# Kernel optimization log

Measured on AMD Instinct MI355X. Metric: run time of the kernel, lower is better.

## Reference

```python
import jax, jax.numpy as jnp
import numpy as np

B, S, E, H, L = 8, 1024, 1024, 16, 2
D = E // H
EPS = 1e-5
THRESH = 0.5


def layer_norm(x, g, b):
    mu = x.mean(-1, keepdims=True)
    var = ((x - mu) ** 2).mean(-1, keepdims=True)
    return (x - mu) * jax.lax.rsqrt(var + EPS) * g + b


def mha(x, w_in, w_out):
    # x: [B,S,E]; w_in: [3E,E]; w_out: [E,E] (no biases, PyTorch MultiheadAttention bias=False)
    qkv = x @ w_in.T  # [B,S,3E]
    q, k, v = jnp.split(qkv, 3, axis=-1)
    q = q.reshape(q.shape[0], q.shape[1], H, D).transpose(0, 2, 1, 3)
    k = k.reshape(k.shape[0], k.shape[1], H, D).transpose(0, 2, 1, 3)
    v = v.reshape(v.shape[0], v.shape[1], H, D).transpose(0, 2, 1, 3)
    scores = jnp.einsum('bhqd,bhkd->bhqk', q, k) / jnp.sqrt(jnp.float32(D)).astype(x.dtype)
    attn = jax.nn.softmax(scores, axis=-1)
    out = jnp.einsum('bhqk,bhkd->bhqd', attn, v)
    out = out.transpose(0, 2, 1, 3).reshape(x.shape[0], x.shape[1], E)
    return out @ w_out.T


def thinking_layer(x, w_in, w_out, ffn1, ffn2, g1, b1, g2, b2):
    x = layer_norm(x + mha(x, w_in, w_out), g1, b1)
    h = jax.nn.gelu(x @ ffn1.T, approximate=False) @ ffn2.T
    return layer_norm(x + h, g2, b2)


def setup_inputs() -> dict:
    key = jax.random.key(0)
    ks = jax.random.split(key, 8)
    s = jnp.float32(0.02)
    return {
        'x': jax.random.normal(ks[0], (B, S, E), jnp.float32),
        'w_in': jax.random.normal(ks[1], (L, 3 * E, E), jnp.float32) * s,
        'w_out': jax.random.normal(ks[2], (L, E, E), jnp.float32) * s,
        'ffn_w1': jax.random.normal(ks[3], (L, 4 * E, E), jnp.float32) * s,
        'ffn_w2': jax.random.normal(ks[4], (L, E, 4 * E), jnp.float32) * s,
        'ln1_g': jnp.ones((L, E), jnp.float32),
        'ln1_b': jnp.zeros((L, E), jnp.float32),
        'ln2_g': jnp.ones((L, E), jnp.float32),
        'ln2_b': jnp.zeros((L, E), jnp.float32),
        'ce_w1': jax.random.normal(ks[5], (E // 4, E), jnp.float32) * s,
        'ce_b1': jnp.zeros((E // 4,), jnp.float32),
        'ce_w2': jax.random.normal(ks[6], (1, E // 4), jnp.float32) * s,
        'ce_b2': jnp.zeros((1,), jnp.float32),
        'fast_w': jax.random.normal(ks[7], (E, E), jnp.float32) * s,
    }


def reference(x, w_in, w_out, ffn_w1, ffn_w2, ln1_g, ln1_b, ln2_g, ln2_b,
              ce_w1, ce_b1, ce_w2, ce_b2, fast_w):
    # complexity estimator: mean-pool -> MLP -> logit per batch element
    pooled = x.mean(axis=1)                                   # [B,E]
    h = jax.nn.relu(pooled @ ce_w1.T + ce_b1)                 # [B,E/4]
    logits = (h @ ce_w2.T + ce_b2).squeeze(-1)                # [B]
    probs = jax.nn.sigmoid(logits)
    mode = (probs > THRESH)                                   # eval-mode deterministic routing

    # thinking path (System 2): L stacked attention+FFN layers
    t = x
    for i in range(L):
        t = thinking_layer(t, w_in[i], w_out[i], ffn_w1[i], ffn_w2[i],
                           ln1_g[i], ln1_b[i], ln2_g[i], ln2_b[i])

    # fast path (System 1)
    fast = jax.nn.gelu(x @ fast_w.T, approximate=False)

    out = jnp.where(mode[:, None, None], t, fast)
    mode_f = mode.astype(x.dtype)
    return out, probs, mode_f, mode_f.mean()
```

## Files before the change

kernel.cpp:

```cpp
#include <hip/hip_runtime.h>
#include <cstdint>
#include <cstddef>

#define Bsz 8
#define Ssz 1024
#define Esz 1024
#define Hn  16
#define Dh  64
#define OUT_PROBS 8388608
#define OUT_MODE  8388616
#define OUT_MEAN  8388624

typedef unsigned short u16;
typedef __attribute__((ext_vector_type(8))) __bf16 bf16x8;
typedef __attribute__((ext_vector_type(4))) float  floatx4;

__device__ __forceinline__ float bf2f(u16 u){ return __uint_as_float(((unsigned)u)<<16); }
__device__ __forceinline__ u16 f2bf(float f){
  unsigned u = __float_as_uint(f);
  u += 0x7fffu + ((u>>16)&1u);
  return (u16)(u>>16);
}
__device__ __forceinline__ void unpack2(unsigned u, float& lo, float& hi){
  lo = __uint_as_float(u<<16);
  hi = __uint_as_float(u & 0xffff0000u);
}
__device__ __forceinline__ unsigned pack2(float lo, float hi){
  return (unsigned)f2bf(lo) | ((unsigned)f2bf(hi)<<16);
}
__device__ __forceinline__ void async16(const void* g, void* l){
  __builtin_amdgcn_global_load_lds((const __attribute__((address_space(1))) void*)g,
                                   (__attribute__((address_space(3))) void*)l, 16, 0, 0);
}
__device__ __forceinline__ float gelu_exact(float x){
  return 0.5f*x*(1.0f + erff(x*0.70710678118654752f));
}

__global__ __launch_bounds__(256)
void f2b_kernel(const float* __restrict__ src, u16* __restrict__ dst, int n8)
{
  const int i = blockIdx.x*256 + threadIdx.x;
  if(i >= n8) return;
  float4 a = ((const float4*)src)[2*i];
  float4 b = ((const float4*)src)[2*i+1];
  uint4 w;
  w.x = pack2(a.x, a.y); w.y = pack2(a.z, a.w);
  w.z = pack2(b.x, b.y); w.w = pack2(b.z, b.w);
  ((uint4*)dst)[i] = w;
}

template<int EPI, int SKIP>
__global__ __launch_bounds__(256, 2)
void gemm_bt(const u16* __restrict__ A, const u16* __restrict__ W,
             void* __restrict__ Cv, const u16* __restrict__ R,
             const float* __restrict__ modes, int N, int K)
{
  const int m0 = blockIdx.x * 128;
  if(SKIP == 1 && modes[m0 >> 10] == 0.0f) return;
  if(SKIP == 2 && modes[m0 >> 10] != 0.0f) return;

  __shared__ __align__(16) u16 AsLo[128*32];
  __shared__ __align__(16) u16 AsHi[128*32];
  __shared__ __align__(16) u16 BsLo[128*32];
  __shared__ __align__(16) u16 BsHi[128*32];

  const int tid  = threadIdx.x;
  const int wave = tid >> 6;
  const int lane = tid & 63;
  const int q    = lane >> 4;
  const int r16  = lane & 15;
  const int wm   = (wave >> 1) * 64;
  const int wn   = (wave & 1) * 64;
  const int n0   = blockIdx.y * 128;

  floatx4 acc[4][4];
  #pragma unroll
  for(int i=0;i<4;i++)
    #pragma unroll
    for(int j=0;j<4;j++){ floatx4 z = {0.f,0.f,0.f,0.f}; acc[i][j] = z; }

  const int row0 = tid >> 2;
  const int kc   = (tid & 3) * 8;

  for(int k0 = 0; k0 < K; k0 += 64){
    __syncthreads();
    async16(A + (size_t)(m0 + row0     )*K + k0 + kc,      AsLo + wave*512);
    async16(A + (size_t)(m0 + row0 + 64)*K + k0 + kc,      AsLo + 2048 + wave*512);
    async16(A + (size_t)(m0 + row0     )*K + k0 + 32 + kc, AsHi + wave*512);
    async16(A + (size_t)(m0 + row0 + 64)*K + k0 + 32 + kc, AsHi + 2048 + wave*512);
    async16(W + (size_t)(n0 + row0     )*K + k0 + kc,      BsLo + wave*512);
    async16(W + (size_t)(n0 + row0 + 64)*K + k0 + kc,      BsLo + 2048 + wave*512);
    async16(W + (size_t)(n0 + row0     )*K + k0 + 32 + kc, BsHi + wave*512);
    async16(W + (size_t)(n0 + row0 + 64)*K + k0 + 32 + kc, BsHi + 2048 + wave*512);
    __syncthreads();

    {
      bf16x8 af[4], bfr[4];
      #pragma unroll
      for(int i=0;i<4;i++){
        af[i]  = *(const bf16x8*)&AsLo[(wm + i*16 + r16)*32 + q*8];
        bfr[i] = *(const bf16x8*)&BsLo[(wn + i*16 + r16)*32 + q*8];
      }
      #pragma unroll
      for(int i=0;i<4;i++)
        #pragma unroll
        for(int j=0;j<4;j++)
          acc[i][j] = __builtin_amdgcn_mfma_f32_16x16x32_bf16(af[i], bfr[j], acc[i][j], 0, 0, 0);
    }
    {
      bf16x8 af[4], bfr[4];
      #pragma unroll
      for(int i=0;i<4;i++){
        af[i]  = *(const bf16x8*)&AsHi[(wm + i*16 + r16)*32 + q*8];
        bfr[i] = *(const bf16x8*)&BsHi[(wn + i*16 + r16)*32 + q*8];
      }
      #pragma unroll
      for(int i=0;i<4;i++)
        #pragma unroll
        for(int j=0;j<4;j++)
          acc[i][j] = __builtin_amdgcn_mfma_f32_16x16x32_bf16(af[i], bfr[j], acc[i][j], 0, 0, 0);
    }
  }

  #pragma unroll
  for(int i=0;i<4;i++){
    const int row = m0 + wm + i*16 + q*4;
    #pragma unroll
    for(int j=0;j<4;j++){
      const int col = n0 + wn + j*16 + r16;
      #pragma unroll
      for(int r=0;r<4;r++){
        float v = acc[i][j][r];
        const size_t idx = (size_t)(row + r)*N + col;
        if(EPI == 1) v += bf2f(R[idx]);
        if(EPI == 2 || EPI == 3) v = gelu_exact(v);
        if(EPI == 3) ((float*)Cv)[idx] = v;
        else         ((u16*)Cv)[idx] = f2bf(v);
      }
    }
  }
}

#define PSTR 136
__global__ __launch_bounds__(256, 2)
void attn_kernel(const u16* __restrict__ qkv, u16* __restrict__ out,
                 const float* __restrict__ modes)
{
  const int bh = blockIdx.x & 127;
  const int b  = bh >> 4;
  if(modes[b] == 0.0f) return;

  __shared__ __align__(16) u16 Qs[2*64*32];
  __shared__ __align__(16) u16 Ks[2*128*32];
  __shared__ __align__(16) u16 Vt[64*PSTR];
  __shared__ __align__(16) u16 Ps[64*PSTR];
  __shared__ float lsump[2][64];

  const int tid = threadIdx.x;
  const int w   = tid >> 6;
  const int lane= tid & 63;
  const int q   = lane >> 4;
  const int r16 = lane & 15;

  const int qt = blockIdx.x >> 7;
  const int h  = bh & 15;
  const int q0 = qt * 64;

  const u16* qbase = qkv + (size_t)(b*Ssz)*3072;

  {
    const int r = tid >> 2;
    const int c = (tid & 3) * 8;
    #pragma unroll
    for(int half=0; half<2; half++)
      async16(qbase + (size_t)(q0 + r)*3072 + h*64 + half*32 + c,
              &Qs[half*2048 + w*512]);
  }

  const int wm  = (w >> 1) * 32;
  const int wnS = (w & 1) * 64;
  const int wnO = (w & 1) * 32;

  floatx4 acc_o[2][2];
  #pragma unroll
  for(int i=0;i<2;i++)
    #pragma unroll
    for(int j=0;j<2;j++){ floatx4 z={0.f,0.f,0.f,0.f}; acc_o[i][j]=z; }
  float ps[2][4] = {{0.f,0.f,0.f,0.f},{0.f,0.f,0.f,0.f}};

  for(int ck=0; ck<8; ck++){
    const int k0 = ck*128;
    __syncthreads();
    {
      const int r = tid >> 2;
      const int c = (tid & 3) * 8;
      #pragma unroll
      for(int half=0; half<2; half++)
        #pragma unroll
        for(int g=0; g<2; g++)
          async16(qbase + (size_t)(k0 + g*64 + r)*3072 + 1024 + h*64 + half*32 + c,
                  &Ks[half*4096 + g*2048 + w*512]);
    }
    {
      const int kp = tid >> 2;
      const int dg = tid & 3;
      const uint4* v0 = (const uint4*)(qbase + (size_t)(k0 + 2*kp    )*3072 + 2048 + h*64 + dg*16);
      const uint4* v1 = (const uint4*)(qbase + (size_t)(k0 + 2*kp + 1)*3072 + 2048 + h*64 + dg*16);
      uint4 a0 = v0[0], a1 = v0[1], b0 = v1[0], b1 = v1[1];
      unsigned wa[8] = {a0.x,a0.y,a0.z,a0.w,a1.x,a1.y,a1.z,a1.w};
      unsigned wb[8] = {b0.x,b0.y,b0.z,b0.w,b1.x,b1.y,b1.z,b1.w};
      unsigned* vt32 = (unsigned*)Vt;
      #pragma unroll
      for(int u=0; u<8; u++){
        const int d = dg*16 + u*2;
        vt32[(size_t)d*68 + kp]     = (wa[u] & 0xffffu) | (wb[u] << 16);
        vt32[(size_t)(d+1)*68 + kp] = (wa[u] >> 16) | (wb[u] & 0xffff0000u);
      }
    }
    __syncthreads();

    floatx4 accS[2][4];
    #pragma unroll
    for(int i=0;i<2;i++)
      #pragma unroll
      for(int j=0;j<4;j++){ floatx4 z={0.f,0.f,0.f,0.f}; accS[i][j]=z; }
    #pragma unroll
    for(int half=0; half<2; half++){
      bf16x8 af[2], bf[4];
      #pragma unroll
      for(int i=0;i<2;i++)
        af[i] = *(const bf16x8*)&Qs[half*2048 + (wm + i*16 + r16)*32 + q*8];
      #pragma unroll
      for(int j=0;j<4;j++)
        bf[j] = *(const bf16x8*)&Ks[half*4096 + (wnS + j*16 + r16)*32 + q*8];
      #pragma unroll
      for(int i=0;i<2;i++)
        #pragma unroll
        for(int j=0;j<4;j++)
          accS[i][j] = __builtin_amdgcn_mfma_f32_16x16x32_bf16(af[i], bf[j], accS[i][j], 0,0,0);
    }
    #pragma unroll
    for(int i=0;i<2;i++)
      #pragma unroll
      for(int j=0;j<4;j++)
        #pragma unroll
        for(int r=0;r<4;r++){
          const float p = __expf(accS[i][j][r] * 0.125f);
          ps[i][r] += p;
          Ps[(size_t)(wm + i*16 + q*4 + r)*PSTR + wnS + j*16 + r16] = f2bf(p);
        }
    __syncthreads();

    #pragma unroll
    for(int ks=0; ks<4; ks++){
      bf16x8 ap[2], bp[2];
      #pragma unroll
      for(int i=0;i<2;i++)
        ap[i] = *(const bf16x8*)&Ps[(size_t)(wm + i*16 + r16)*PSTR + ks*32 + q*8];
      #pragma unroll
      for(int j=0;j<2;j++)
        bp[j] = *(const bf16x8*)&Vt[(size_t)(wnO + j*16 + r16)*PSTR + ks*32 + q*8];
      #pragma unroll
      for(int i=0;i<2;i++)
        #pragma unroll
        for(int j=0;j<2;j++)
          acc_o[i][j] = __builtin_amdgcn_mfma_f32_16x16x32_bf16(ap[i], bp[j], acc_o[i][j], 0,0,0);
    }
  }

  #pragma unroll
  for(int i=0;i<2;i++)
    #pragma unroll
    for(int r=0;r<4;r++){
      float v = ps[i][r];
      v += __shfl_xor(v, 1, 64);
      v += __shfl_xor(v, 2, 64);
      v += __shfl_xor(v, 4, 64);
      v += __shfl_xor(v, 8, 64);
      ps[i][r] = v;
    }
  if(r16 == 0){
    #pragma unroll
    for(int i=0;i<2;i++)
      #pragma unroll
      for(int r=0;r<4;r++)
        lsump[w & 1][wm + i*16 + q*4 + r] = ps[i][r];
  }
  __syncthreads();

  #pragma unroll
  for(int i=0;i<2;i++)
    #pragma unroll
    for(int r=0;r<4;r++){
      const int row = wm + i*16 + q*4 + r;
      const float inv = 1.0f / (lsump[0][row] + lsump[1][row]);
      #pragma unroll
      for(int j=0;j<2;j++){
        const int col = h*64 + wnO + j*16 + r16;
        out[(size_t)(b*Ssz + q0 + row)*Esz + col] = f2bf(acc_o[i][j][r] * inv);
      }
    }
}

template<int FIN>
__global__ __launch_bounds__(256)
void ln_kernel(const u16* __restrict__ X, const float* __restrict__ G,
               const float* __restrict__ Bi, u16* __restrict__ Y,
               const float* __restrict__ modes, float* __restrict__ outp)
{
  const int row = blockIdx.x;
  if(modes[row >> 10] == 0.0f) return;
  const int tid = threadIdx.x;
  const int wave = tid >> 6, lane = tid & 63;

  uint2 u = ((const uint2*)(X + (size_t)row*Esz))[tid];
  float x0,x1,x2,x3;
  unpack2(u.x, x0, x1); unpack2(u.y, x2, x3);
  float s  = x0+x1+x2+x3;
  float ss = x0*x0 + x1*x1 + x2*x2 + x3*x3;
  #pragma unroll
  for(int off=32; off; off>>=1){
    s  += __shfl_down(s,  off, 64);
    ss += __shfl_down(ss, off, 64);
  }
  __shared__ float rs[4], rss[4], bc[2];
  if(lane == 0){ rs[wave] = s; rss[wave] = ss; }
  __syncthreads();
  if(tid == 0){
    float S  = rs[0]+rs[1]+rs[2]+rs[3];
    float SS = rss[0]+rss[1]+rss[2]+rss[3];
    float mu  = S * (1.0f/1024.0f);
    float var = SS * (1.0f/1024.0f) - mu*mu;
    bc[0] = mu; bc[1] = 1.0f/sqrtf(var + 1e-5f);
  }
  __syncthreads();
  const float mu = bc[0], inv = bc[1];
  float4 g4 = ((const float4*)G)[tid];
  float4 b4 = ((const float4*)Bi)[tid];
  if(FIN){
    float4 o;
    o.x = (x0-mu)*inv*g4.x + b4.x;
    o.y = (x1-mu)*inv*g4.y + b4.y;
    o.z = (x2-mu)*inv*g4.z + b4.z;
    o.w = (x3-mu)*inv*g4.w + b4.w;
    ((float4*)(outp + (size_t)row*Esz))[tid] = o;
  } else {
    uint2 w;
    w.x = pack2((x0-mu)*inv*g4.x + b4.x, (x1-mu)*inv*g4.y + b4.y);
    w.y = pack2((x2-mu)*inv*g4.z + b4.z, (x3-mu)*inv*g4.w + b4.w);
    ((uint2*)(Y + (size_t)row*Esz))[tid] = w;
  }
}

__global__ __launch_bounds__(256)
void pool1_kernel(const float* __restrict__ x, float* __restrict__ part)
{
  const int b = blockIdx.x, tc = blockIdx.y;
  const int e4 = threadIdx.x;
  const float* p = x + (size_t)(b*Ssz + tc*32)*Esz + e4*4;
  float4 s = {0.f,0.f,0.f,0.f};
  for(int t=0; t<32; t++){
    float4 v = *(const float4*)(p + (size_t)t*Esz);
    s.x += v.x; s.y += v.y; s.z += v.z; s.w += v.w;
  }
  ((float4*)(part + (size_t)(b*32 + tc)*Esz))[e4] = s;
}

__global__ void ce1_kernel(const float* __restrict__ part, const float* __restrict__ w1,
                           const float* __restrict__ b1, float* __restrict__ hbuf)
{
  __shared__ float pl[1024];
  const int b = blockIdx.x, n = threadIdx.x;
  for(int i = threadIdx.x; i < 1024; i += 256){
    float s = 0.f;
    for(int tc=0; tc<32; tc++) s += part[(size_t)(b*32 + tc)*Esz + i];
    pl[i] = s * (1.0f/1024.0f);
  }
  __syncthreads();
  const float* wr = w1 + (size_t)n*1024;
  float s = 0.f;
  for(int k=0; k<1024; k++) s += pl[k]*wr[k];
  s += b1[n];
  hbuf[b*256 + n] = fmaxf(s, 0.f);
}

__global__ void ce2_kernel(const float* __restrict__ hbuf, const float* __restrict__ w2,
                           const float* __restrict__ b2, float* __restrict__ modes,
                           float* __restrict__ outp)
{
  const int tid = threadIdx.x;
  const int b = tid >> 5, i = tid & 31;
  float s = 0.f;
  for(int k=i; k<256; k+=32) s += hbuf[b*256 + k] * w2[k];
  #pragma unroll
  for(int off=16; off; off>>=1) s += __shfl_down(s, off, 32);
  __shared__ float md[8];
  if(i == 0){
    const float logit = s + b2[0];
    const float prob = 1.0f/(1.0f + expf(-logit));
    const float m = prob > 0.5f ? 1.0f : 0.0f;
    modes[b] = m; md[b] = m;
    outp[OUT_PROBS + b] = prob;
    outp[OUT_MODE  + b] = m;
  }
  __syncthreads();
  if(tid == 0){
    float acc = 0.f;
    for(int k=0;k<8;k++) acc += md[k];
    outp[OUT_MEAN] = acc * 0.125f;
  }
}

extern "C" void kernel_launch(void* const* d_in, const int* in_sizes, int n_in,
                              void* d_out, int out_size, void* d_ws, size_t ws_size,
                              hipStream_t stream)
{
  const float* x      = (const float*)d_in[0];
  const float* w_in   = (const float*)d_in[1];
  const float* w_out  = (const float*)d_in[2];
  const float* ffn_w1 = (const float*)d_in[3];
  const float* ffn_w2 = (const float*)d_in[4];
  const float* ln1_g  = (const float*)d_in[5];
  const float* ln1_b  = (const float*)d_in[6];
  const float* ln2_g  = (const float*)d_in[7];
  const float* ln2_b  = (const float*)d_in[8];
  const float* ce_w1  = (const float*)d_in[9];
  const float* ce_b1  = (const float*)d_in[10];
  const float* ce_w2  = (const float*)d_in[11];
  const float* ce_b2  = (const float*)d_in[12];
  const float* fast_w = (const float*)d_in[13];
  float* out = (float*)d_out;

  u16* x_bf     = (u16*)d_ws;
  u16* w_in_bf  = x_bf    + (size_t)8192*1024;
  u16* w_out_bf = w_in_bf + (size_t)2*3072*1024;
  u16* ffn1_bf  = w_out_bf+ (size_t)2*1024*1024;
  u16* ffn2_bf  = ffn1_bf + (size_t)2*4096*1024;
  u16* fast_bf  = ffn2_bf + (size_t)2*1024*4096;
  u16* big      = fast_bf + (size_t)1024*1024;
  u16* attn     = big     + (size_t)8192*4096;
  u16* resid    = attn    + (size_t)8192*1024;
  u16* bufA     = resid   + (size_t)8192*1024;
  u16* bufB     = bufA    + (size_t)8192*1024;
  float* part   = (float*)(bufB + (size_t)8192*1024);
  float* hbuf   = part + (size_t)8*32*1024;
  float* modes  = hbuf + 2048;
  const size_t need = (size_t)((char*)(modes + 8) - (char*)d_ws);
  if(ws_size < need) return;

  u16* qkv  = big;
  u16* hmid = big;

  f2b_kernel<<<4096, 256, 0, stream>>>(x,      x_bf,     8192*1024/8);
  f2b_kernel<<<3072, 256, 0, stream>>>(w_in,   w_in_bf,  2*3072*1024/8);
  f2b_kernel<<<1024, 256, 0, stream>>>(w_out,  w_out_bf, 2*1024*1024/8);
  f2b_kernel<<<4096, 256, 0, stream>>>(ffn_w1, ffn1_bf,  2*4096*1024/8);
  f2b_kernel<<<4096, 256, 0, stream>>>(ffn_w2, ffn2_bf,  2*4096*1024/8);
  f2b_kernel<<< 512, 256, 0, stream>>>(fast_w, fast_bf,  1024*1024/8);

  pool1_kernel<<<dim3(8,32), 256, 0, stream>>>(x, part);
  ce1_kernel<<<8, 256, 0, stream>>>(part, ce_w1, ce_b1, hbuf);
  ce2_kernel<<<1, 256, 0, stream>>>(hbuf, ce_w2, ce_b2, modes, out);

  const u16* t = x_bf;
  for(int l=0; l<2; l++){
    gemm_bt<0,1><<<dim3(64,24), 256, 0, stream>>>(t, w_in_bf + (size_t)l*3072*1024, qkv, nullptr, modes, 3072, 1024);
    attn_kernel<<<2048, 256, 0, stream>>>(qkv, attn, modes);
    gemm_bt<1,1><<<dim3(64, 8), 256, 0, stream>>>(attn, w_out_bf + (size_t)l*1024*1024, resid, t, modes, 1024, 1024);
    ln_kernel<0><<<8192, 256, 0, stream>>>(resid, ln1_g + l*1024, ln1_b + l*1024, bufA, modes, nullptr);
    gemm_bt<2,1><<<dim3(64,32), 256, 0, stream>>>(bufA, ffn1_bf + (size_t)l*4096*1024, hmid, nullptr, modes, 4096, 1024);
    gemm_bt<1,1><<<dim3(64, 8), 256, 0, stream>>>(hmid, ffn2_bf + (size_t)l*1024*4096, resid, bufA, modes, 1024, 4096);
    if(l == 0)
      ln_kernel<0><<<8192, 256, 0, stream>>>(resid, ln2_g + l*1024, ln2_b + l*1024, bufB, modes, nullptr);
    else
      ln_kernel<1><<<8192, 256, 0, stream>>>(resid, ln2_g + l*1024, ln2_b + l*1024, nullptr, modes, out);
    t = bufB;
  }

  gemm_bt<3,2><<<dim3(64, 8), 256, 0, stream>>>(x_bf, fast_bf, out, nullptr, modes, 1024, 1024);
}
```

Measured before the change: 958.7 us.

## Shrink attention key tile, hoist Q fragments, and batch fp32-to-bf16 conversions

The attention kernel now processes keys in 64-row chunks instead of 128, with smaller shared K/V/P buffers. It also keeps Q fragments in registers across the loop and raises launch bounds to 4 blocks per CU for higher occupancy. The six separate fp32-to-bf16 conversion launches are merged into a single multi-segment kernel to cut launch overhead. The trade-off is twice as many loop iterations and barriers in attention, and a per-thread segment lookup in the conversion kernel.

After: 913.9 us. 4.7% less time.

```diff
diff --git a/kernel.cpp b/kernel.cpp
--- a/kernel.cpp
+++ b/kernel.cpp
@@ -36,17 +36,26 @@
   return 0.5f*x*(1.0f + erff(x*0.70710678118654752f));
 }
 
+struct F2B {
+  const float* s[6];
+  u16* d[6];
+  unsigned end[6];
+};
+
 __global__ __launch_bounds__(256)
-void f2b_kernel(const float* __restrict__ src, u16* __restrict__ dst, int n8)
-{
-  const int i = blockIdx.x*256 + threadIdx.x;
-  if(i >= n8) return;
-  float4 a = ((const float4*)src)[2*i];
-  float4 b = ((const float4*)src)[2*i+1];
+void f2b_multi(F2B p)
+{
+  const unsigned i = blockIdx.x*256 + threadIdx.x;
+  int k = 0;
+  #pragma unroll
+  for(int t=0; t<5; t++) if(i >= p.end[t]) k = t+1;
+  const unsigned j = i - (k ? p.end[k-1] : 0);
+  float4 a = ((const float4*)p.s[k])[2*j];
+  float4 b = ((const float4*)p.s[k])[2*j+1];
   uint4 w;
   w.x = pack2(a.x, a.y); w.y = pack2(a.z, a.w);
   w.z = pack2(b.x, b.y); w.w = pack2(b.z, b.w);
-  ((uint4*)dst)[i] = w;
+  ((uint4*)p.d[k])[j] = w;
 }
 
 template<int EPI, int SKIP>
@@ -141,8 +150,9 @@
   }
 }
 
-#define PSTR 136
-__global__ __launch_bounds__(256, 2)
+#define VSTR 68
+#define PSTR 72
+__global__ __launch_bounds__(256, 4)
 void attn_kernel(const u16* __restrict__ qkv, u16* __restrict__ out,
                  const float* __restrict__ modes)
 {
@@ -151,8 +161,8 @@
   if(modes[b] == 0.0f) return;
 
   __shared__ __align__(16) u16 Qs[2*64*32];
-  __shared__ __align__(16) u16 Ks[2*128*32];
-  __shared__ __align__(16) u16 Vt[64*PSTR];
+  __shared__ __align__(16) u16 Ks[2*64*32];
+  __shared__ __align__(16) u16 Vt[64*VSTR];
   __shared__ __align__(16) u16 Ps[64*PSTR];
   __shared__ float lsump[2][64];
 
@@ -168,18 +178,25 @@
 
   const u16* qbase = qkv + (size_t)(b*Ssz)*3072;
 
-  {
-    const int r = tid >> 2;
-    const int c = (tid & 3) * 8;
-    #pragma unroll
-    for(int half=0; half<2; half++)
-      async16(qbase + (size_t)(q0 + r)*3072 + h*64 + half*32 + c,
-              &Qs[half*2048 + w*512]);
-  }
+  const int sr = tid >> 2;
+  const int sc = (tid & 3) * 8;
+
+  #pragma unroll
+  for(int half=0; half<2; half++)
+    async16(qbase + (size_t)(q0 + sr)*3072 + h*64 + half*32 + sc,
+            &Qs[half*2048 + w*512]);
+  __syncthreads();
 
   const int wm  = (w >> 1) * 32;
-  const int wnS = (w & 1) * 64;
+  const int wnS = (w & 1) * 32;
   const int wnO = (w & 1) * 32;
+
+  bf16x8 qf[2][2];
+  #pragma unroll
+  for(int half=0; half<2; half++)
+    #pragma unroll
+    for(int i=0;i<2;i++)
+      qf[half][i] = *(const bf16x8*)&Qs[half*2048 + (wm + i*16 + r16)*32 + q*8];
 
   floatx4 acc_o[2][2];
   #pragma unroll
@@ -188,61 +205,52 @@
     for(int j=0;j<2;j++){ floatx4 z={0.f,0.f,0.f,0.f}; acc_o[i][j]=z; }
   float ps[2][4] = {{0.f,0.f,0.f,0.f},{0.f,0.f,0.f,0.f}};
 
-  for(int ck=0; ck<8; ck++){
-    const int k0 = ck*128;
+  const int kp = tid & 31;
+  const int dg = tid >> 5;
+
+  for(int ck=0; ck<16; ck++){
+    const int k0 = ck*64;
     __syncthreads();
+    #pragma unroll
+    for(int half=0; half<2; half++)
+      async16(qbase + (size_t)(k0 + sr)*3072 + 1024 + h*64 + half*32 + sc,
+              &Ks[half*2048 + w*512]);
     {
-      const int r = tid >> 2;
-      const int c = (tid & 3) * 8;
-      #pragma unroll
-      for(int half=0; half<2; half++)
-        #pragma unroll
-        for(int g=0; g<2; g++)
-          async16(qbase + (size_t)(k0 + g*64 + r)*3072 + 1024 + h*64 + half*32 + c,
-                  &Ks[half*4096 + g*2048 + w*512]);
-    }
-    {
-      const int kp = tid >> 2;
-      const int dg = tid & 3;
-      const uint4* v0 = (const uint4*)(qbase + (size_t)(k0 + 2*kp    )*3072 + 2048 + h*64 + dg*16);
-      const uint4* v1 = (const uint4*)(qbase + (size_t)(k0 + 2*kp + 1)*3072 + 2048 + h*64 + dg*16);
-      uint4 a0 = v0[0], a1 = v0[1], b0 = v1[0], b1 = v1[1];
-      unsigned wa[8] = {a0.x,a0.y,a0.z,a0.w,a1.x,a1.y,a1.z,a1.w};
-      unsigned wb[8] = {b0.x,b0.y,b0.z,b0.w,b1.x,b1.y,b1.z,b1.w};
+      const uint4 va = *(const uint4*)(qbase + (size_t)(k0 + 2*kp    )*3072 + 2048 + h*64 + dg*8);
+      const uint4 vb = *(const uint4*)(qbase + (size_t)(k0 + 2*kp + 1)*3072 + 2048 + h*64 + dg*8);
+      unsigned wa[4] = {va.x,va.y,va.z,va.w};
+      unsigned wb[4] = {vb.x,vb.y,vb.z,vb.w};
       unsigned* vt32 = (unsigned*)Vt;
       #pragma unroll
-      for(int u=0; u<8; u++){
-        const int d = dg*16 + u*2;
-        vt32[(size_t)d*68 + kp]     = (wa[u] & 0xffffu) | (wb[u] << 16);
-        vt32[(size_t)(d+1)*68 + kp] = (wa[u] >> 16) | (wb[u] & 0xffff0000u);
+      for(int u=0; u<4; u++){
+        const int d0 = dg*8 + 2*u;
+        vt32[(size_t)d0*34 + kp]     = (wa[u] & 0xffffu) | (wb[u] << 16);
+        vt32[(size_t)(d0+1)*34 + kp] = (wa[u] >> 16) | (wb[u] & 0xffff0000u);
       }
     }
     __syncthreads();
 
-    floatx4 accS[2][4];
+    floatx4 accS[2][2];
     #pragma unroll
     for(int i=0;i<2;i++)
       #pragma unroll
-      for(int j=0;j<4;j++){ floatx4 z={0.f,0.f,0.f,0.f}; accS[i][j]=z; }
+      for(int j=0;j<2;j++){ floatx4 z={0.f,0.f,0.f,0.f}; accS[i][j]=z; }
     #pragma unroll
     for(int half=0; half<2; half++){
-      bf16x8 af[2], bf[4];
-      #pragma unroll
-      for(int i=0;i<2;i++)
-        af[i] = *(const bf16x8*)&Qs[half*2048 + (wm + i*16 + r16)*32 + q*8];
-      #pragma unroll
-      for(int j=0;j<4;j++)
-        bf[j] = *(const bf16x8*)&Ks[half*4096 + (wnS + j*16 + r16)*32 + q*8];
+      bf16x8 bf[2];
+      #pragma unroll
+      for(int j=0;j<2;j++)
+        bf[j] = *(const bf16x8*)&Ks[half*2048 + (wnS + j*16 + r16)*32 + q*8];
       #pragma unroll
       for(int i=0;i<2;i++)
         #pragma unroll
-        for(int j=0;j<4;j++)
-          accS[i][j] = __builtin_amdgcn_mfma_f32_16x16x32_bf16(af[i], bf[j], accS[i][j], 0,0,0);
+        for(int j=0;j<2;j++)
+          accS[i][j] = __builtin_amdgcn_mfma_f32_16x16x32_bf16(qf[half][i], bf[j], accS[i][j], 0,0,0);
     }
     #pragma unroll
     for(int i=0;i<2;i++)
       #pragma unroll
-      for(int j=0;j<4;j++)
+      for(int j=0;j<2;j++)
         #pragma unroll
         for(int r=0;r<4;r++){
           const float p = __expf(accS[i][j][r] * 0.125f);
@@ -252,14 +260,14 @@
     __syncthreads();
 
     #pragma unroll
-    for(int ks=0; ks<4; ks++){
+    for(int ks=0; ks<2; ks++){
       bf16x8 ap[2], bp[2];
       #pragma unroll
       for(int i=0;i<2;i++)
         ap[i] = *(const bf16x8*)&Ps[(size_t)(wm + i*16 + r16)*PSTR + ks*32 + q*8];
       #pragma unroll
       for(int j=0;j<2;j++)
-        bp[j] = *(const bf16x8*)&Vt[(size_t)(wnO + j*16 + r16)*PSTR + ks*32 + q*8];
+        bp[j] = *(const bf16x8*)&Vt[(size_t)(wnO + j*16 + r16)*VSTR + ks*32 + q*8];
       #pragma unroll
       for(int i=0;i<2;i++)
         #pragma unroll
@@ -451,12 +459,18 @@
   u16* qkv  = big;
   u16* hmid = big;
 
-  f2b_kernel<<<4096, 256, 0, stream>>>(x,      x_bf,     8192*1024/8);
-  f2b_kernel<<<3072, 256, 0, stream>>>(w_in,   w_in_bf,  2*3072*1024/8);
-  f2b_kernel<<<1024, 256, 0, stream>>>(w_out,  w_out_bf, 2*1024*1024/8);
-  f2b_kernel<<<4096, 256, 0, stream>>>(ffn_w1, ffn1_bf,  2*4096*1024/8);
-  f2b_kernel<<<4096, 256, 0, stream>>>(ffn_w2, ffn2_bf,  2*4096*1024/8);
-  f2b_kernel<<< 512, 256, 0, stream>>>(fast_w, fast_bf,  1024*1024/8);
+  {
+    F2B p;
+    p.s[0]=x;      p.d[0]=x_bf;     unsigned n0c = 8192u*1024u/8u;
+    p.s[1]=w_in;   p.d[1]=w_in_bf;  unsigned n1c = 2u*3072u*1024u/8u;
+    p.s[2]=w_out;  p.d[2]=w_out_bf; unsigned n2c = 2u*1024u*1024u/8u;
+    p.s[3]=ffn_w1; p.d[3]=ffn1_bf;  unsigned n3c = 2u*4096u*1024u/8u;
+    p.s[4]=ffn_w2; p.d[4]=ffn2_bf;  unsigned n4c = 2u*4096u*1024u/8u;
+    p.s[5]=fast_w; p.d[5]=fast_bf;  unsigned n5c = 1024u*1024u/8u;
+    p.end[0]=n0c; p.end[1]=p.end[0]+n1c; p.end[2]=p.end[1]+n2c;
+    p.end[3]=p.end[2]+n3c; p.end[4]=p.end[3]+n4c; p.end[5]=p.end[4]+n5c;
+    f2b_multi<<<p.end[5]/256, 256, 0, stream>>>(p);
+  }
 
   pool1_kernel<<<dim3(8,32), 256, 0, stream>>>(x, part);
   ce1_kernel<<<8, 256, 0, stream>>>(part, ce_w1, ce_b1, hbuf);
```
